# Performance work log

Measured on AMD Instinct MI355X. Metric: run time of the kernel, lower is better.

The kernel has to match this reference:

```python
import jax, jax.numpy as jnp
import numpy as np
import math

D_MODEL = 1024
N_HEADS = 16
DEPTH = D_MODEL // N_HEADS
ROPE_BASE = 10000.0
LS_INIT = 1e-05


def _rope_cos_sin(seq_len, depth, dtype=jnp.float32):
    inv_freq = 1.0 / (ROPE_BASE ** (jnp.arange(0, depth, 2, dtype=jnp.float32) / depth))
    t = jnp.arange(seq_len, dtype=jnp.float32)
    freqs = jnp.einsum('i,j->ij', t, inv_freq)          # [S, depth/2]
    emb = jnp.concatenate([freqs, freqs], axis=-1)       # [S, depth]
    return emb.astype(dtype).cos()[None, None], emb.astype(dtype).sin()[None, None]  # wrong order fixed below


def rope_cos_sin(seq_len, depth):
    inv_freq = 1.0 / (ROPE_BASE ** (jnp.arange(0, depth, 2, dtype=jnp.float32) / depth))
    t = jnp.arange(seq_len, dtype=jnp.float32)
    freqs = jnp.einsum('i,j->ij', t, inv_freq)          # [S, depth/2]
    emb = jnp.concatenate([freqs, freqs], axis=-1)       # [S, depth]
    return jnp.cos(emb)[None, None], jnp.sin(emb)[None, None]  # [1,1,S,depth]


def rotate_half(x):
    x1, x2 = jnp.split(x, 2, axis=-1)
    return jnp.concatenate([-x2, x1], axis=-1)


def setup_inputs() -> dict:
    key = jax.random.key(0)
    ks = jax.random.split(key, 6)
    B, S, D = 2, 2048, D_MODEL
    s = 1.0 / math.sqrt(D)
    return {
        'query': jax.random.normal(ks[0], (B, S, D), dtype=jnp.float32),
        'Wq': jax.random.normal(ks[1], (D, D), dtype=jnp.float32) * s,
        'bq': jnp.zeros((D,), jnp.float32),
        'Wk': jax.random.normal(ks[2], (D, D), dtype=jnp.float32) * s,
        'bk': jnp.zeros((D,), jnp.float32),
        'Wv': jax.random.normal(ks[3], (D, D), dtype=jnp.float32) * s,
        'bv': jnp.zeros((D,), jnp.float32),
        'Wo': jax.random.normal(ks[4], (D, D), dtype=jnp.float32) * s,
        'bo': jnp.zeros((D,), jnp.float32),
        'gamma': jnp.full((D,), LS_INIT, jnp.float32),
    }


def reference(query, Wq, bq, Wk, bk, Wv, bv, Wo, bo, gamma):
    B, S, D = query.shape
    H, dh = N_HEADS, DEPTH

    def split_heads(x):  # [B,S,D] -> [B,H,S,dh]
        return x.reshape(B, S, H, dh).transpose(0, 2, 1, 3)

    # torch Linear: x @ W.T + b, W is [out,in]
    q = split_heads(query @ Wq.T + bq)
    k = split_heads(query @ Wk.T + bk)
    v = split_heads(query @ Wv.T + bv)

    cos, sin = rope_cos_sin(S, dh)  # [1,1,S,dh]
    q = q * cos + rotate_half(q) * sin
    k = k * cos + rotate_half(k) * sin

    logits = jnp.einsum('bhqd,bhkd->bhqk', q, k) / math.sqrt(dh)
    attn = jax.nn.softmax(logits, axis=-1)          # dropout = identity (eval)
    out = jnp.einsum('bhqk,bhkd->bhqd', attn, v)    # [B,H,S,dh]
    out = out.transpose(0, 2, 1, 3).reshape(B, S, D)
    out = out @ Wo.T + bo
    return gamma * out
```

## Files before the change

### kernel.cpp

```cpp
#include <hip/hip_runtime.h>
#include <hip/hip_bf16.h>
#include <math.h>

typedef __bf16 bf16_t;
typedef __bf16 bf16x8 __attribute__((ext_vector_type(8)));
typedef float floatx4 __attribute__((ext_vector_type(4)));

#define SC_QK 0.18033688011112042f

__device__ __forceinline__ float fast_exp2(float x) {
#if __has_builtin(__builtin_amdgcn_exp2f)
  return __builtin_amdgcn_exp2f(x);
#else
  return exp2f(x);
#endif
}

__device__ __forceinline__ void async_load16(const bf16_t* g, bf16_t* l) {
  __builtin_amdgcn_global_load_lds(
      (__attribute__((address_space(1))) void*)(void*)g,
      (__attribute__((address_space(3))) void*)l, 16, 0, 0);
}

__global__ __launch_bounds__(256) void convert_kernel(
    const float* __restrict__ query, const float* __restrict__ Wq,
    const float* __restrict__ Wk, const float* __restrict__ Wv,
    const float* __restrict__ Wo, bf16_t* __restrict__ Xbf,
    bf16_t* __restrict__ Wqkv, bf16_t* __restrict__ Wobf) {
  long base = ((long)blockIdx.x * 256 + threadIdx.x) * 4;
  const float* src;
  bf16_t* dst;
  long off;
  if (base < 4194304L)      { src = query; dst = Xbf;             off = base; }
  else if (base < 5242880L) { src = Wq;    dst = Wqkv;            off = base - 4194304L; }
  else if (base < 6291456L) { src = Wk;    dst = Wqkv + 1048576;  off = base - 5242880L; }
  else if (base < 7340032L) { src = Wv;    dst = Wqkv + 2097152;  off = base - 6291456L; }
  else                      { src = Wo;    dst = Wobf;            off = base - 7340032L; }
  float4 v = *reinterpret_cast<const float4*>(src + off);
  dst[off + 0] = (bf16_t)v.x;
  dst[off + 1] = (bf16_t)v.y;
  dst[off + 2] = (bf16_t)v.z;
  dst[off + 3] = (bf16_t)v.w;
}

__device__ __forceinline__ void gemm_tile_async(const bf16_t* __restrict__ A,
                                                const bf16_t* __restrict__ Bn,
                                                int m0, int n0,
                                                floatx4 acc[4][4]) {
  __shared__ __align__(16) bf16_t As[128 * 32];
  __shared__ __align__(16) bf16_t Bs[128 * 32];
  const int tid = threadIdx.x;
  const int lane = tid & 63;
  const int wave = tid >> 6;
  const int wm = (wave >> 1) * 64;
  const int wn = (wave & 1) * 64;
  const int lr = lane & 15;
  const int lq = lane >> 4;
  const int srow = lane >> 2;
  const int scol = (lane & 3) * 8;

  for (int kk = 0; kk < 1024; kk += 32) {
    __syncthreads();
#pragma unroll
    for (int u = 0; u < 2; u++) {
      int t = wave * 2 + u;
      int row = t * 16 + srow;
      async_load16(A + (size_t)(m0 + row) * 1024 + kk + scol, &As[t * 512]);
      async_load16(Bn + (size_t)(n0 + row) * 1024 + kk + scol, &Bs[t * 512]);
    }
    __syncthreads();
    bf16x8 af[4], bfr[4];
#pragma unroll
    for (int i = 0; i < 4; i++)
      af[i] = *reinterpret_cast<const bf16x8*>(&As[(wm + i * 16 + lr) * 32 + lq * 8]);
#pragma unroll
    for (int j = 0; j < 4; j++)
      bfr[j] = *reinterpret_cast<const bf16x8*>(&Bs[(wn + j * 16 + lr) * 32 + lq * 8]);
#pragma unroll
    for (int i = 0; i < 4; i++)
#pragma unroll
      for (int j = 0; j < 4; j++)
        acc[i][j] = __builtin_amdgcn_mfma_f32_16x16x32_bf16(af[i], bfr[j],
                                                            acc[i][j], 0, 0, 0);
  }
}

__global__ __launch_bounds__(256, 3) void qkv_kernel(
    const bf16_t* __restrict__ Xbf, const bf16_t* __restrict__ Wqkv,
    const float* __restrict__ bq, const float* __restrict__ bk,
    const float* __restrict__ bv, bf16_t* __restrict__ Qbuf,
    bf16_t* __restrict__ Kbuf, bf16_t* __restrict__ Vt) {
  const int m0 = blockIdx.x * 128;
  const int n0 = blockIdx.y * 128;
  const int z = blockIdx.z;
  floatx4 acc[4][4];
  floatx4 zero4 = {0.f, 0.f, 0.f, 0.f};
#pragma unroll
  for (int i = 0; i < 4; i++)
#pragma unroll
    for (int j = 0; j < 4; j++) acc[i][j] = zero4;

  gemm_tile_async(Xbf, Wqkv + (size_t)z * 1048576, m0, n0, acc);

  const int lane = threadIdx.x & 63;
  const int wave = threadIdx.x >> 6;
  const int wm = (wave >> 1) * 64;
  const int wn = (wave & 1) * 64;
  const int lr = lane & 15;
  const int lq = lane >> 4;
  const int h = (n0 + wn) >> 6;

  if (z == 2) {
#pragma unroll
    for (int i = 0; i < 4; i++)
#pragma unroll
      for (int j = 0; j < 4; j++)
#pragma unroll
        for (int r = 0; r < 4; r++) {
          int m = m0 + wm + i * 16 + lq * 4 + r;
          int n = n0 + wn + j * 16 + lr;
          float v = acc[i][j][r] + bv[n];
          int b = m >> 11, s = m & 2047;
          int d = n & 63;
          Vt[((size_t)(b * 16 + h) * 64 + d) * 2048 + s] = (bf16_t)v;
        }
  } else {
    bf16_t* dst = (z == 0) ? Qbuf : Kbuf;
    const float* bias = (z == 0) ? bq : bk;
    const float sc = (z == 0) ? SC_QK : 1.0f;
#pragma unroll
    for (int i = 0; i < 4; i++)
#pragma unroll
      for (int r = 0; r < 4; r++) {
        int m = m0 + wm + i * 16 + lq * 4 + r;
        int b = m >> 11, s = m & 2047;
        size_t rowbase = ((size_t)(b * 16 + h) * 2048 + s) * 64;
#pragma unroll
        for (int jj = 0; jj < 2; jj++) {
          int d1 = jj * 16 + lr;
          int n1 = n0 + wn + d1;
          float x1 = acc[i][jj][r] + bias[n1];
          float x2 = acc[i][jj + 2][r] + bias[n1 + 32];
          float invf = __expf(-(float)d1 * 0.28782313662425576f);
          float ang = (float)s * invf;
          float c, sn;
          sincosf(ang, &sn, &c);
          dst[rowbase + d1]      = (bf16_t)((x1 * c - x2 * sn) * sc);
          dst[rowbase + d1 + 32] = (bf16_t)((x2 * c + x1 * sn) * sc);
        }
      }
  }
}

__global__ __launch_bounds__(512, 4) void attn_kernel(
    const bf16_t* __restrict__ Qbuf, const bf16_t* __restrict__ Kbuf,
    const bf16_t* __restrict__ Vt, bf16_t* __restrict__ Ctx) {
  __shared__ __align__(16) bf16_t Ks[128 * 64];
  __shared__ __align__(16) bf16_t Vs[64 * 128];
  __shared__ __align__(16) bf16_t Ps[8][16][136];
  const int tid = threadIdx.x;
  const int lane = tid & 63;
  const int w = tid >> 6;
  const int lr = lane & 15;
  const int lq = lane >> 4;
  const int q0 = blockIdx.x * 128;
  const int bh = blockIdx.y;
  const size_t hb = (size_t)bh * (2048 * 64);

  const bf16_t* qp = Qbuf + hb + (size_t)(q0 + w * 16 + lr) * 64 + lq * 8;
  bf16x8 aq0 = *reinterpret_cast<const bf16x8*>(qp);
  bf16x8 aq1 = *reinterpret_cast<const bf16x8*>(qp + 32);

  floatx4 o[4];
  float mr[4], lsum[4];
  floatx4 zero4 = {0.f, 0.f, 0.f, 0.f};
#pragma unroll
  for (int i = 0; i < 4; i++) o[i] = zero4;
#pragma unroll
  for (int i = 0; i < 4; i++) { mr[i] = -1e30f; lsum[i] = 0.f; }

  const int krow_l = lane >> 3;
  const int kblk_l = lane & 7;
  const int vrow_l = lane >> 4;
  const int vblk_l = lane & 15;

  for (int kt = 0; kt < 16; kt++) {
    const int k0 = kt * 128;
    __syncthreads();
#pragma unroll
    for (int u = 0; u < 2; u++) {
      int t = w * 2 + u;
      {
        int r = t * 8 + krow_l;
        int c = kblk_l ^ (r & 7);
        async_load16(Kbuf + hb + (size_t)(k0 + r) * 64 + c * 8, &Ks[t * 512]);
      }
      {
        int d = t * 4 + vrow_l;
        int c = vblk_l ^ (d & 15);
        async_load16(Vt + hb + (size_t)d * 2048 + k0 + c * 8, &Vs[t * 512]);
      }
    }
    __syncthreads();

    floatx4 sf[8];
#pragma unroll
    for (int nt = 0; nt < 8; nt++) {
      int krow = nt * 16 + lr;
      bf16x8 b0 = *reinterpret_cast<const bf16x8*>(
          &Ks[krow * 64 + (lq ^ (krow & 7)) * 8]);
      bf16x8 b1 = *reinterpret_cast<const bf16x8*>(
          &Ks[krow * 64 + (((4 + lq)) ^ (krow & 7)) * 8]);
      floatx4 z4 = zero4;
      z4 = __builtin_amdgcn_mfma_f32_16x16x32_bf16(aq0, b0, z4, 0, 0, 0);
      z4 = __builtin_amdgcn_mfma_f32_16x16x32_bf16(aq1, b1, z4, 0, 0, 0);
      sf[nt] = z4;
    }

    float mn_[4], al[4];
#pragma unroll
    for (int r = 0; r < 4; r++) {
      float m = sf[0][r];
#pragma unroll
      for (int nt = 1; nt < 8; nt++) m = fmaxf(m, sf[nt][r]);
      m = fmaxf(m, __shfl_xor(m, 1, 64));
      m = fmaxf(m, __shfl_xor(m, 2, 64));
      m = fmaxf(m, __shfl_xor(m, 4, 64));
      m = fmaxf(m, __shfl_xor(m, 8, 64));
      mn_[r] = fmaxf(mr[r], m);
      al[r] = fast_exp2(mr[r] - mn_[r]);
      mr[r] = mn_[r];
    }
    float ls[4] = {0.f, 0.f, 0.f, 0.f};
#pragma unroll
    for (int nt = 0; nt < 8; nt++)
#pragma unroll
      for (int r = 0; r < 4; r++) {
        float p = fast_exp2(sf[nt][r] - mn_[r]);
        ls[r] += p;
        Ps[w][lq * 4 + r][nt * 16 + lr] = (bf16_t)p;
      }
#pragma unroll
    for (int r = 0; r < 4; r++) {
      float t = ls[r];
      t += __shfl_xor(t, 1, 64);
      t += __shfl_xor(t, 2, 64);
      t += __shfl_xor(t, 4, 64);
      t += __shfl_xor(t, 8, 64);
      lsum[r] = lsum[r] * al[r] + t;
      o[0][r] *= al[r];
      o[1][r] *= al[r];
      o[2][r] *= al[r];
      o[3][r] *= al[r];
    }

#pragma unroll
    for (int kk = 0; kk < 4; kk++) {
      bf16x8 ap = *reinterpret_cast<const bf16x8*>(&Ps[w][lr][kk * 32 + lq * 8]);
#pragma unroll
      for (int dt = 0; dt < 4; dt++) {
        int d = dt * 16 + lr;
        bf16x8 bv_ = *reinterpret_cast<const bf16x8*>(
            &Vs[d * 128 + (((kk * 4 + lq)) ^ (d & 15)) * 8]);
        o[dt] = __builtin_amdgcn_mfma_f32_16x16x32_bf16(ap, bv_, o[dt], 0, 0, 0);
      }
    }
  }

  const int b = bh >> 4;
  const int h = bh & 15;
#pragma unroll
  for (int r = 0; r < 4; r++) {
    float inv_l = 1.0f / lsum[r];
    int srow = q0 + w * 16 + lq * 4 + r;
#pragma unroll
    for (int dt = 0; dt < 4; dt++) {
      Ctx[((size_t)(b * 2048 + srow)) * 1024 + h * 64 + dt * 16 + lr] =
          (bf16_t)(o[dt][r] * inv_l);
    }
  }
}

__global__ __launch_bounds__(256, 3) void oproj_kernel(
    const bf16_t* __restrict__ Ctx, const bf16_t* __restrict__ Wobf,
    const float* __restrict__ bo, const float* __restrict__ gamma,
    float* __restrict__ out) {
  const int m0 = blockIdx.x * 128;
  const int n0 = blockIdx.y * 128;
  floatx4 acc[4][4];
  floatx4 zero4 = {0.f, 0.f, 0.f, 0.f};
#pragma unroll
  for (int i = 0; i < 4; i++)
#pragma unroll
    for (int j = 0; j < 4; j++) acc[i][j] = zero4;

  gemm_tile_async(Ctx, Wobf, m0, n0, acc);

  const int lane = threadIdx.x & 63;
  const int wave = threadIdx.x >> 6;
  const int wm = (wave >> 1) * 64;
  const int wn = (wave & 1) * 64;
  const int lr = lane & 15;
  const int lq = lane >> 4;
#pragma unroll
  for (int i = 0; i < 4; i++)
#pragma unroll
    for (int j = 0; j < 4; j++)
#pragma unroll
      for (int r = 0; r < 4; r++) {
        int m = m0 + wm + i * 16 + lq * 4 + r;
        int n = n0 + wn + j * 16 + lr;
        out[(size_t)m * 1024 + n] = gamma[n] * (acc[i][j][r] + bo[n]);
      }
}

extern "C" void kernel_launch(void* const* d_in, const int* in_sizes, int n_in,
                              void* d_out, int out_size, void* d_ws,
                              size_t ws_size, hipStream_t stream) {
  const float* query = (const float*)d_in[0];
  const float* Wq = (const float*)d_in[1];
  const float* bq = (const float*)d_in[2];
  const float* Wk = (const float*)d_in[3];
  const float* bk = (const float*)d_in[4];
  const float* Wv = (const float*)d_in[5];
  const float* bv = (const float*)d_in[6];
  const float* Wo = (const float*)d_in[7];
  const float* bo = (const float*)d_in[8];
  const float* gamma = (const float*)d_in[9];
  float* out = (float*)d_out;

  char* ws = (char*)d_ws;
  bf16_t* Xbf  = (bf16_t*)(ws);
  bf16_t* Wqkv = (bf16_t*)(ws + (8ull << 20));
  bf16_t* Wobf = (bf16_t*)(ws + (14ull << 20));
  bf16_t* Qbuf = (bf16_t*)(ws + (16ull << 20));
  bf16_t* Kbuf = (bf16_t*)(ws + (24ull << 20));
  bf16_t* Vt   = (bf16_t*)(ws + (32ull << 20));
  bf16_t* Ctx  = (bf16_t*)(ws + (40ull << 20));

  convert_kernel<<<dim3(8192), dim3(256), 0, stream>>>(query, Wq, Wk, Wv, Wo,
                                                       Xbf, Wqkv, Wobf);
  qkv_kernel<<<dim3(32, 8, 3), dim3(256), 0, stream>>>(Xbf, Wqkv, bq, bk, bv,
                                                       Qbuf, Kbuf, Vt);
  attn_kernel<<<dim3(16, 32), dim3(512), 0, stream>>>(Qbuf, Kbuf, Vt, Ctx);
  oproj_kernel<<<dim3(32, 8), dim3(256), 0, stream>>>(Ctx, Wobf, bo, gamma, out);
}
```

Before: 224.7 us.

## Restructure attention to keep P in registers and precompute RoPE table

The attention kernel now computes the transposed scores (K·Q) so each lane already holds the P fragment that a 16x16x16 MFMA needs for the PV product. This removes the shared-memory round trip for P. Each of 4 waves now handles 32 query rows (two groups), so every K/V fragment read from LDS feeds two query groups, and the block shrinks to 256 threads. RoPE cos/sin values are precomputed into a table by a separate small kernel, which removes the per-element expf and sincosf from the QKV epilogue. The table is placed in the Ctx workspace region; this works only because qkv finishes reading it before attention writes Ctx.

```diff
diff --git a/kernel.cpp b/kernel.cpp
--- a/kernel.cpp
+++ b/kernel.cpp
@@ -4,6 +4,8 @@
 
 typedef __bf16 bf16_t;
 typedef __bf16 bf16x8 __attribute__((ext_vector_type(8)));
+typedef __bf16 bf16x4 __attribute__((ext_vector_type(4)));
+typedef short short4v __attribute__((ext_vector_type(4)));
 typedef float floatx4 __attribute__((ext_vector_type(4)));
 
 #define SC_QK 0.18033688011112042f
@@ -20,6 +22,20 @@
   __builtin_amdgcn_global_load_lds(
       (__attribute__((address_space(1))) void*)(void*)g,
       (__attribute__((address_space(3))) void*)l, 16, 0, 0);
+}
+
+__device__ __forceinline__ floatx4 mfma_pv(bf16x4 vfrag, bf16x4 pfrag,
+                                           floatx4 acc) {
+#if __has_builtin(__builtin_amdgcn_mfma_f32_16x16x16bf16_1k)
+  return __builtin_amdgcn_mfma_f32_16x16x16bf16_1k(
+      __builtin_bit_cast(short4v, vfrag), __builtin_bit_cast(short4v, pfrag),
+      acc, 0, 0, 0);
+#else
+  const bf16_t z = (bf16_t)0.0f;
+  bf16x8 a = {vfrag[0], vfrag[1], vfrag[2], vfrag[3], z, z, z, z};
+  bf16x8 b = {pfrag[0], pfrag[1], pfrag[2], pfrag[3], z, z, z, z};
+  return __builtin_amdgcn_mfma_f32_16x16x32_bf16(a, b, acc, 0, 0, 0);
+#endif
 }
 
 __global__ __launch_bounds__(256) void convert_kernel(
@@ -43,6 +59,18 @@
   dst[off + 3] = (bf16_t)v.w;
 }
 
+__global__ __launch_bounds__(256) void rope_tab_kernel(float* __restrict__ tab) {
+  int idx = blockIdx.x * 256 + threadIdx.x;
+  int s = idx >> 5;
+  int p = idx & 31;
+  float invf = __expf(-(float)p * 0.28782313662425576f);
+  float ang = (float)s * invf;
+  float c, sn;
+  sincosf(ang, &sn, &c);
+  tab[idx] = c;
+  tab[65536 + idx] = sn;
+}
+
 __device__ __forceinline__ void gemm_tile_async(const bf16_t* __restrict__ A,
                                                 const bf16_t* __restrict__ Bn,
                                                 int m0, int n0,
@@ -88,8 +116,9 @@
 __global__ __launch_bounds__(256, 3) void qkv_kernel(
     const bf16_t* __restrict__ Xbf, const bf16_t* __restrict__ Wqkv,
     const float* __restrict__ bq, const float* __restrict__ bk,
-    const float* __restrict__ bv, bf16_t* __restrict__ Qbuf,
-    bf16_t* __restrict__ Kbuf, bf16_t* __restrict__ Vt) {
+    const float* __restrict__ bv, const float* __restrict__ Tab,
+    bf16_t* __restrict__ Qbuf, bf16_t* __restrict__ Kbuf,
+    bf16_t* __restrict__ Vt) {
   const int m0 = blockIdx.x * 128;
   const int n0 = blockIdx.y * 128;
   const int z = blockIdx.z;
@@ -141,10 +170,8 @@
           int n1 = n0 + wn + d1;
           float x1 = acc[i][jj][r] + bias[n1];
           float x2 = acc[i][jj + 2][r] + bias[n1 + 32];
-          float invf = __expf(-(float)d1 * 0.28782313662425576f);
-          float ang = (float)s * invf;
-          float c, sn;
-          sincosf(ang, &sn, &c);
+          float c = Tab[s * 32 + d1];
+          float sn = Tab[65536 + s * 32 + d1];
           dst[rowbase + d1]      = (bf16_t)((x1 * c - x2 * sn) * sc);
           dst[rowbase + d1 + 32] = (bf16_t)((x2 * c + x1 * sn) * sc);
         }
@@ -152,12 +179,12 @@
   }
 }
 
-__global__ __launch_bounds__(512, 4) void attn_kernel(
+__global__ __launch_bounds__(256, 3) void attn_kernel(
     const bf16_t* __restrict__ Qbuf, const bf16_t* __restrict__ Kbuf,
     const bf16_t* __restrict__ Vt, bf16_t* __restrict__ Ctx) {
-  __shared__ __align__(16) bf16_t Ks[128 * 64];
-  __shared__ __align__(16) bf16_t Vs[64 * 128];
-  __shared__ __align__(16) bf16_t Ps[8][16][136];
+  __shared__ __align__(16) bf16_t Sh[16384];
+  bf16_t* Ks = Sh;
+  bf16_t* Vs = Sh + 8192;
   const int tid = threadIdx.x;
   const int lane = tid & 63;
   const int w = tid >> 6;
@@ -166,117 +193,134 @@
   const int q0 = blockIdx.x * 128;
   const int bh = blockIdx.y;
   const size_t hb = (size_t)bh * (2048 * 64);
-
-  const bf16_t* qp = Qbuf + hb + (size_t)(q0 + w * 16 + lr) * 64 + lq * 8;
-  bf16x8 aq0 = *reinterpret_cast<const bf16x8*>(qp);
-  bf16x8 aq1 = *reinterpret_cast<const bf16x8*>(qp + 32);
-
-  floatx4 o[4];
-  float mr[4], lsum[4];
+  const int qw = q0 + w * 32;
+
+  bf16x8 qf[2][2];
+#pragma unroll
+  for (int g = 0; g < 2; g++) {
+    const bf16_t* qp = Qbuf + hb + (size_t)(qw + g * 16 + lr) * 64 + lq * 8;
+    qf[g][0] = *reinterpret_cast<const bf16x8*>(qp);
+    qf[g][1] = *reinterpret_cast<const bf16x8*>(qp + 32);
+  }
+
+  floatx4 o[2][4];
+  float mr[2], lsum[2];
   floatx4 zero4 = {0.f, 0.f, 0.f, 0.f};
 #pragma unroll
-  for (int i = 0; i < 4; i++) o[i] = zero4;
-#pragma unroll
-  for (int i = 0; i < 4; i++) { mr[i] = -1e30f; lsum[i] = 0.f; }
-
-  const int krow_l = lane >> 3;
-  const int kblk_l = lane & 7;
-  const int vrow_l = lane >> 4;
-  const int vblk_l = lane & 15;
+  for (int g = 0; g < 2; g++) {
+    mr[g] = -1e30f;
+    lsum[g] = 0.f;
+#pragma unroll
+    for (int dt = 0; dt < 4; dt++) o[g][dt] = zero4;
+  }
+
+  const int ksr = lane >> 3;
+  const int ksb = lane & 7;
+  const int vsr = lane >> 4;
+  const int vsb = lane & 15;
 
   for (int kt = 0; kt < 16; kt++) {
     const int k0 = kt * 128;
     __syncthreads();
 #pragma unroll
-    for (int u = 0; u < 2; u++) {
-      int t = w * 2 + u;
+    for (int u = 0; u < 4; u++) {
+      int t = w * 4 + u;
       {
-        int r = t * 8 + krow_l;
-        int c = kblk_l ^ (r & 7);
-        async_load16(Kbuf + hb + (size_t)(k0 + r) * 64 + c * 8, &Ks[t * 512]);
+        int r = t * 8 + ksr;
+        int c = ksb ^ (r & 7);
+        async_load16(Kbuf + hb + (size_t)(k0 + r) * 64 + c * 8, Ks + t * 512);
       }
       {
-        int d = t * 4 + vrow_l;
-        int c = vblk_l ^ (d & 15);
-        async_load16(Vt + hb + (size_t)d * 2048 + k0 + c * 8, &Vs[t * 512]);
+        int d = t * 4 + vsr;
+        int c = vsb ^ (d & 15);
+        async_load16(Vt + hb + (size_t)d * 2048 + k0 + c * 8, Vs + t * 512);
       }
     }
     __syncthreads();
 
-    floatx4 sf[8];
+    floatx4 sf[2][8];
 #pragma unroll
     for (int nt = 0; nt < 8; nt++) {
       int krow = nt * 16 + lr;
-      bf16x8 b0 = *reinterpret_cast<const bf16x8*>(
+      bf16x8 kf0 = *reinterpret_cast<const bf16x8*>(
           &Ks[krow * 64 + (lq ^ (krow & 7)) * 8]);
-      bf16x8 b1 = *reinterpret_cast<const bf16x8*>(
-          &Ks[krow * 64 + (((4 + lq)) ^ (krow & 7)) * 8]);
-      floatx4 z4 = zero4;
-      z4 = __builtin_amdgcn_mfma_f32_16x16x32_bf16(aq0, b0, z4, 0, 0, 0);
-      z4 = __builtin_amdgcn_mfma_f32_16x16x32_bf16(aq1, b1, z4, 0, 0, 0);
-      sf[nt] = z4;
-    }
-
-    float mn_[4], al[4];
-#pragma unroll
-    for (int r = 0; r < 4; r++) {
-      float m = sf[0][r];
-#pragma unroll
-      for (int nt = 1; nt < 8; nt++) m = fmaxf(m, sf[nt][r]);
-      m = fmaxf(m, __shfl_xor(m, 1, 64));
-      m = fmaxf(m, __shfl_xor(m, 2, 64));
-      m = fmaxf(m, __shfl_xor(m, 4, 64));
-      m = fmaxf(m, __shfl_xor(m, 8, 64));
-      mn_[r] = fmaxf(mr[r], m);
-      al[r] = fast_exp2(mr[r] - mn_[r]);
-      mr[r] = mn_[r];
-    }
-    float ls[4] = {0.f, 0.f, 0.f, 0.f};
-#pragma unroll
-    for (int nt = 0; nt < 8; nt++)
-#pragma unroll
-      for (int r = 0; r < 4; r++) {
-        float p = fast_exp2(sf[nt][r] - mn_[r]);
-        ls[r] += p;
-        Ps[w][lq * 4 + r][nt * 16 + lr] = (bf16_t)p;
-      }
-#pragma unroll
-    for (int r = 0; r < 4; r++) {
-      float t = ls[r];
-      t += __shfl_xor(t, 1, 64);
-      t += __shfl_xor(t, 2, 64);
-      t += __shfl_xor(t, 4, 64);
-      t += __shfl_xor(t, 8, 64);
-      lsum[r] = lsum[r] * al[r] + t;
-      o[0][r] *= al[r];
-      o[1][r] *= al[r];
-      o[2][r] *= al[r];
-      o[3][r] *= al[r];
-    }
-
-#pragma unroll
-    for (int kk = 0; kk < 4; kk++) {
-      bf16x8 ap = *reinterpret_cast<const bf16x8*>(&Ps[w][lr][kk * 32 + lq * 8]);
+      bf16x8 kf1 = *reinterpret_cast<const bf16x8*>(
+          &Ks[krow * 64 + ((4 + lq) ^ (krow & 7)) * 8]);
+#pragma unroll
+      for (int g = 0; g < 2; g++) {
+        floatx4 z4 = zero4;
+        z4 = __builtin_amdgcn_mfma_f32_16x16x32_bf16(kf0, qf[g][0], z4, 0, 0, 0);
+        z4 = __builtin_amdgcn_mfma_f32_16x16x32_bf16(kf1, qf[g][1], z4, 0, 0, 0);
+        sf[g][nt] = z4;
+      }
+    }
+
+    float mn_[2], al[2], ls[2];
+#pragma unroll
+    for (int g = 0; g < 2; g++) {
+      floatx4 mv = sf[g][0];
+#pragma unroll
+      for (int nt = 1; nt < 8; nt++) {
+#pragma unroll
+        for (int r = 0; r < 4; r++) mv[r] = fmaxf(mv[r], sf[g][nt][r]);
+      }
+      float m = fmaxf(fmaxf(mv[0], mv[1]), fmaxf(mv[2], mv[3]));
+      m = fmaxf(m, __shfl_xor(m, 16, 64));
+      m = fmaxf(m, __shfl_xor(m, 32, 64));
+      float mn = fmaxf(mr[g], m);
+      al[g] = fast_exp2(mr[g] - mn);
+      mr[g] = mn;
+      mn_[g] = mn;
+      ls[g] = 0.f;
+#pragma unroll
+      for (int dt = 0; dt < 4; dt++) o[g][dt] *= al[g];
+    }
+
+#pragma unroll
+    for (int nt = 0; nt < 8; nt++) {
+      bf16x4 vf[4];
 #pragma unroll
       for (int dt = 0; dt < 4; dt++) {
         int d = dt * 16 + lr;
-        bf16x8 bv_ = *reinterpret_cast<const bf16x8*>(
-            &Vs[d * 128 + (((kk * 4 + lq)) ^ (d & 15)) * 8]);
-        o[dt] = __builtin_amdgcn_mfma_f32_16x16x32_bf16(ap, bv_, o[dt], 0, 0, 0);
-      }
+        int blk = (2 * nt + (lq >> 1)) ^ (d & 15);
+        vf[dt] = *reinterpret_cast<const bf16x4*>(
+            &Vs[d * 128 + blk * 8 + (lq & 1) * 4]);
+      }
+#pragma unroll
+      for (int g = 0; g < 2; g++) {
+        bf16x4 pg;
+#pragma unroll
+        for (int r = 0; r < 4; r++) {
+          float pv = fast_exp2(sf[g][nt][r] - mn_[g]);
+          ls[g] += pv;
+          pg[r] = (bf16_t)pv;
+        }
+#pragma unroll
+        for (int dt = 0; dt < 4; dt++)
+          o[g][dt] = mfma_pv(vf[dt], pg, o[g][dt]);
+      }
+    }
+#pragma unroll
+    for (int g = 0; g < 2; g++) {
+      float t = ls[g];
+      t += __shfl_xor(t, 16, 64);
+      t += __shfl_xor(t, 32, 64);
+      lsum[g] = lsum[g] * al[g] + t;
     }
   }
 
   const int b = bh >> 4;
   const int h = bh & 15;
 #pragma unroll
-  for (int r = 0; r < 4; r++) {
-    float inv_l = 1.0f / lsum[r];
-    int srow = q0 + w * 16 + lq * 4 + r;
+  for (int g = 0; g < 2; g++) {
+    float inv_l = 1.0f / lsum[g];
+    size_t rowb = ((size_t)(b * 2048 + qw + g * 16 + lr)) * 1024 + h * 64;
 #pragma unroll
     for (int dt = 0; dt < 4; dt++) {
-      Ctx[((size_t)(b * 2048 + srow)) * 1024 + h * 64 + dt * 16 + lr] =
-          (bf16_t)(o[dt][r] * inv_l);
+      bf16x4 pk;
+#pragma unroll
+      for (int r = 0; r < 4; r++) pk[r] = (bf16_t)(o[g][dt][r] * inv_l);
+      *reinterpret_cast<bf16x4*>(&Ctx[rowb + dt * 16 + lq * 4]) = pk;
     }
   }
 }
@@ -337,11 +381,13 @@
   bf16_t* Kbuf = (bf16_t*)(ws + (24ull << 20));
   bf16_t* Vt   = (bf16_t*)(ws + (32ull << 20));
   bf16_t* Ctx  = (bf16_t*)(ws + (40ull << 20));
-
+  float*  Tab  = (float*)(ws + (40ull << 20));
+
+  rope_tab_kernel<<<dim3(256), dim3(256), 0, stream>>>(Tab);
   convert_kernel<<<dim3(8192), dim3(256), 0, stream>>>(query, Wq, Wk, Wv, Wo,
                                                        Xbf, Wqkv, Wobf);
   qkv_kernel<<<dim3(32, 8, 3), dim3(256), 0, stream>>>(Xbf, Wqkv, bq, bk, bv,
-                                                       Qbuf, Kbuf, Vt);
-  attn_kernel<<<dim3(16, 32), dim3(512), 0, stream>>>(Qbuf, Kbuf, Vt, Ctx);
+                                                       Tab, Qbuf, Kbuf, Vt);
+  attn_kernel<<<dim3(16, 32), dim3(256), 0, stream>>>(Qbuf, Kbuf, Vt, Ctx);
   oproj_kernel<<<dim3(32, 8), dim3(256), 0, stream>>>(Ctx, Wobf, bo, gamma, out);
 }
```

Result: no change. 221.1 us (-1.6%).
